# Performance work log

Hardware: AMD Instinct MI355X
Metric: run time of the kernel (lower is better)

## Reference

```python
import jax, jax.numpy as jnp
import numpy as np

NUM_NEURONS = 8192
INPUT_SIZE = 512
OUTPUT_SIZE = 512
TAU = 10.0
G = 1.5


def setup_inputs() -> dict:
    key = jax.random.key(0)
    k1, k2, k3, k4, k5 = jax.random.split(key, 5)
    inputs = jax.random.normal(k1, (INPUT_SIZE,), dtype=jnp.float32)
    potentials = jax.random.normal(k2, (1, NUM_NEURONS), dtype=jnp.float32)
    # parameters, matching the torch init scales
    W_in = jax.random.normal(k3, (INPUT_SIZE, NUM_NEURONS), dtype=jnp.float32) * 0.1
    synapses = jax.random.normal(k4, (NUM_NEURONS, NUM_NEURONS), dtype=jnp.float32) / np.sqrt(NUM_NEURONS).astype(np.float32)
    W_out = jax.random.normal(k5, (NUM_NEURONS, OUTPUT_SIZE), dtype=jnp.float32) / np.float32(NUM_NEURONS)
    return {"inputs": inputs, "potentials": potentials, "W_in": W_in,
            "synapses": synapses, "W_out": W_out}


def reference(inputs, potentials, W_in, synapses, W_out):
    # input_map: bias-free linear, then unsqueeze to [1, N]
    drive = (inputs @ W_in)[None, :]                      # [1, N]
    # Neurons: continuous-time leaky integrator (FORCE-style)
    rates = jnp.tanh(potentials)                          # [1, N]
    pot_new = potentials + (-potentials + G * (rates @ synapses) + drive) / TAU
    gen_net = jnp.tanh(pot_new)                           # [1, N]
    # read_out: bias-free linear
    output = gen_net @ W_out                              # [1, output_size]
    return (output, pot_new)
```

## Files before the change

### kernel.cpp

```cpp
#include <hip/hip_runtime.h>
#include <math.h>

#define N_NEU   8192
#define IN_SZ   512
#define OUT_SZ  512
#define N4      (N_NEU / 4)
#define OUT4    (OUT_SZ / 4)
#define KPB     64
#define SYN_TILES (N_NEU / KPB)
#define WIN_TILES (IN_SZ / KPB)
#define TILES     (SYN_TILES + WIN_TILES)
#define K2_KPB  128
#define OTILES  (N_NEU / K2_KPB)
constexpr float TAU_INV = 0.1f;
constexpr float G_GAIN  = 1.5f;

__global__ __launch_bounds__(256)
void accum_kernel(const float* __restrict__ pot,
                  const float* __restrict__ inputs,
                  const float* __restrict__ synapses,
                  const float* __restrict__ W_in,
                  float4* __restrict__ P4,
                  float* __restrict__ out) {
    __shared__ float xs[KPB];
    const int bx = blockIdx.x, by = blockIdx.y;
    const int tid = threadIdx.x;
    const float4* M;
    int k0;
    if (by < SYN_TILES) {
        k0 = by * KPB;
        M  = (const float4*)synapses;
        if (tid < KPB) xs[tid] = G_GAIN * tanhf(pot[k0 + tid]);
    } else {
        k0 = (by - SYN_TILES) * KPB;
        M  = (const float4*)W_in;
        if (tid < KPB) xs[tid] = inputs[k0 + tid];
    }
    if (by == TILES - 1 && tid < 64) out[bx * 64 + tid] = 0.0f;
    __syncthreads();

    const int col4 = bx * 256 + tid;
    const float4* Mp = M + (size_t)k0 * N4 + col4;

    float4 acc = make_float4(0.f, 0.f, 0.f, 0.f);
#pragma unroll 8
    for (int i = 0; i < KPB; ++i) {
        float  s = xs[i];
        float4 m = Mp[(size_t)i * N4];
        acc.x = fmaf(s, m.x, acc.x);
        acc.y = fmaf(s, m.y, acc.y);
        acc.z = fmaf(s, m.z, acc.z);
        acc.w = fmaf(s, m.w, acc.w);
    }
    P4[(size_t)(by * 8 + bx) * 256 + tid] = acc;
}

__global__ __launch_bounds__(128)
void finish_kernel(const float* __restrict__ pot,
                   const float* __restrict__ P,
                   const float* __restrict__ W_out,
                   float* __restrict__ out) {
    const int b = blockIdx.x;
    const int t = threadIdx.x;
    if (b < OTILES) {
        __shared__ float xs[K2_KPB];
        const int k0  = b * K2_KPB;
        const int bx  = k0 >> 10;
        const int off = (k0 & 1023) + t;
        float s = 0.f;
#pragma unroll 8
        for (int by = 0; by < TILES; ++by)
            s += P[(size_t)(by * 8 + bx) * 1024 + off];
        float p  = pot[k0 + t];
        float pn = p + (s - p) * TAU_INV;
        xs[t] = tanhf(pn);
        __syncthreads();

        const float4* Wp = (const float4*)W_out + (size_t)k0 * OUT4 + t;
        float4 acc = make_float4(0.f, 0.f, 0.f, 0.f);
#pragma unroll 8
        for (int i = 0; i < K2_KPB; ++i) {
            float  sx = xs[i];
            float4 m  = Wp[(size_t)i * OUT4];
            acc.x = fmaf(sx, m.x, acc.x);
            acc.y = fmaf(sx, m.y, acc.y);
            acc.z = fmaf(sx, m.z, acc.z);
            acc.w = fmaf(sx, m.w, acc.w);
        }
        float* op = out + (size_t)t * 4;
        atomicAdd(op + 0, acc.x);
        atomicAdd(op + 1, acc.y);
        atomicAdd(op + 2, acc.z);
        atomicAdd(op + 3, acc.w);
    } else {
        const int j   = (b - OTILES) * 128 + t;
        const int bx  = j >> 10;
        const int off = j & 1023;
        float s = 0.f;
#pragma unroll 8
        for (int by = 0; by < TILES; ++by)
            s += P[(size_t)(by * 8 + bx) * 1024 + off];
        float p  = pot[j];
        float pn = p + (s - p) * TAU_INV;
        out[OUT_SZ + j] = pn;
    }
}

extern "C" void kernel_launch(void* const* d_in, const int* in_sizes, int n_in,
                              void* d_out, int out_size, void* d_ws, size_t ws_size,
                              hipStream_t stream) {
    const float* inputs   = (const float*)d_in[0];
    const float* pot      = (const float*)d_in[1];
    const float* W_in     = (const float*)d_in[2];
    const float* synapses = (const float*)d_in[3];
    const float* W_out    = (const float*)d_in[4];

    float* out = (float*)d_out;
    float* P   = (float*)d_ws;

    accum_kernel<<<dim3(8, TILES), dim3(256), 0, stream>>>(
        pot, inputs, synapses, W_in, (float4*)P, out);

    finish_kernel<<<dim3(OTILES + N_NEU / 128), dim3(128), 0, stream>>>(
        pot, P, W_out, out);
}
```

Before: 407.7 us.

## Reduce matvec partials with atomics into output instead of workspace buffer

The accumulate kernel now atomically adds its per-tile partial sums straight into the pot_new region of the output, instead of writing them to a workspace buffer that the finish kernel later re-reads. A separate zero kernel clears the output first. The finish kernel is simplified to read the reduced sums, write pot_new, and do the readout matvec. Tile sizes change as well: 128 rows per accumulate tile and 64 per readout tile. This removes the partial-buffer round trip and the strided reduction loop, at the cost of many contended float atomics and an extra launch. The larger accumulate tile also halves the number of blocks streaming the synapse matrix.

```diff
diff --git a/kernel.cpp b/kernel.cpp
--- a/kernel.cpp
+++ b/kernel.cpp
@@ -6,21 +6,25 @@
 #define OUT_SZ  512
 #define N4      (N_NEU / 4)
 #define OUT4    (OUT_SZ / 4)
-#define KPB     64
+#define KPB     128
 #define SYN_TILES (N_NEU / KPB)
 #define WIN_TILES (IN_SZ / KPB)
 #define TILES     (SYN_TILES + WIN_TILES)
-#define K2_KPB  128
+#define K2_KPB  64
 #define OTILES  (N_NEU / K2_KPB)
 constexpr float TAU_INV = 0.1f;
 constexpr float G_GAIN  = 1.5f;
+
+__global__ __launch_bounds__(256)
+void zero_kernel(float* __restrict__ out) {
+    out[blockIdx.x * 256 + threadIdx.x] = 0.0f;
+}
 
 __global__ __launch_bounds__(256)
 void accum_kernel(const float* __restrict__ pot,
                   const float* __restrict__ inputs,
                   const float* __restrict__ synapses,
                   const float* __restrict__ W_in,
-                  float4* __restrict__ P4,
                   float* __restrict__ out) {
     __shared__ float xs[KPB];
     const int bx = blockIdx.x, by = blockIdx.y;
@@ -36,7 +40,6 @@
         M  = (const float4*)W_in;
         if (tid < KPB) xs[tid] = inputs[k0 + tid];
     }
-    if (by == TILES - 1 && tid < 64) out[bx * 64 + tid] = 0.0f;
     __syncthreads();
 
     const int col4 = bx * 256 + tid;
@@ -52,58 +55,47 @@
         acc.z = fmaf(s, m.z, acc.z);
         acc.w = fmaf(s, m.w, acc.w);
     }
-    P4[(size_t)(by * 8 + bx) * 256 + tid] = acc;
+    float* op = out + OUT_SZ + (size_t)col4 * 4;
+    atomicAdd(op + 0, acc.x);
+    atomicAdd(op + 1, acc.y);
+    atomicAdd(op + 2, acc.z);
+    atomicAdd(op + 3, acc.w);
 }
 
 __global__ __launch_bounds__(128)
 void finish_kernel(const float* __restrict__ pot,
-                   const float* __restrict__ P,
                    const float* __restrict__ W_out,
                    float* __restrict__ out) {
+    __shared__ float xs[K2_KPB];
     const int b = blockIdx.x;
     const int t = threadIdx.x;
-    if (b < OTILES) {
-        __shared__ float xs[K2_KPB];
-        const int k0  = b * K2_KPB;
-        const int bx  = k0 >> 10;
-        const int off = (k0 & 1023) + t;
-        float s = 0.f;
-#pragma unroll 8
-        for (int by = 0; by < TILES; ++by)
-            s += P[(size_t)(by * 8 + bx) * 1024 + off];
+    const int k0 = b * K2_KPB;
+
+    if (t < K2_KPB) {
+        float s  = out[OUT_SZ + k0 + t];
         float p  = pot[k0 + t];
         float pn = p + (s - p) * TAU_INV;
+        out[OUT_SZ + k0 + t] = pn;
         xs[t] = tanhf(pn);
-        __syncthreads();
+    }
+    __syncthreads();
 
-        const float4* Wp = (const float4*)W_out + (size_t)k0 * OUT4 + t;
-        float4 acc = make_float4(0.f, 0.f, 0.f, 0.f);
+    const float4* Wp = (const float4*)W_out + (size_t)k0 * OUT4 + t;
+    float4 acc = make_float4(0.f, 0.f, 0.f, 0.f);
 #pragma unroll 8
-        for (int i = 0; i < K2_KPB; ++i) {
-            float  sx = xs[i];
-            float4 m  = Wp[(size_t)i * OUT4];
-            acc.x = fmaf(sx, m.x, acc.x);
-            acc.y = fmaf(sx, m.y, acc.y);
-            acc.z = fmaf(sx, m.z, acc.z);
-            acc.w = fmaf(sx, m.w, acc.w);
-        }
-        float* op = out + (size_t)t * 4;
-        atomicAdd(op + 0, acc.x);
-        atomicAdd(op + 1, acc.y);
-        atomicAdd(op + 2, acc.z);
-        atomicAdd(op + 3, acc.w);
-    } else {
-        const int j   = (b - OTILES) * 128 + t;
-        const int bx  = j >> 10;
-        const int off = j & 1023;
-        float s = 0.f;
-#pragma unroll 8
-        for (int by = 0; by < TILES; ++by)
-            s += P[(size_t)(by * 8 + bx) * 1024 + off];
-        float p  = pot[j];
-        float pn = p + (s - p) * TAU_INV;
-        out[OUT_SZ + j] = pn;
+    for (int i = 0; i < K2_KPB; ++i) {
+        float  sx = xs[i];
+        float4 m  = Wp[(size_t)i * OUT4];
+        acc.x = fmaf(sx, m.x, acc.x);
+        acc.y = fmaf(sx, m.y, acc.y);
+        acc.z = fmaf(sx, m.z, acc.z);
+        acc.w = fmaf(sx, m.w, acc.w);
     }
+    float* op = out + (size_t)t * 4;
+    atomicAdd(op + 0, acc.x);
+    atomicAdd(op + 1, acc.y);
+    atomicAdd(op + 2, acc.z);
+    atomicAdd(op + 3, acc.w);
 }
 
 extern "C" void kernel_launch(void* const* d_in, const int* in_sizes, int n_in,
@@ -116,11 +108,12 @@
     const float* W_out    = (const float*)d_in[4];
 
     float* out = (float*)d_out;
-    float* P   = (float*)d_ws;
+    (void)d_ws; (void)ws_size;
+
+    zero_kernel<<<dim3((OUT_SZ + N_NEU) / 256), dim3(256), 0, stream>>>(out);
 
     accum_kernel<<<dim3(8, TILES), dim3(256), 0, stream>>>(
-        pot, inputs, synapses, W_in, (float4*)P, out);
+        pot, inputs, synapses, W_in, out);
 
-    finish_kernel<<<dim3(OTILES + N_NEU / 128), dim3(128), 0, stream>>>(
-        pot, P, W_out, out);
+    finish_kernel<<<dim3(OTILES), dim3(128), 0, stream>>>(pot, W_out, out);
 }
```

Measured after the change: 404.6 us. About the same (-0.7%).
